# Performance work log

Measured on AMD Instinct MI355X. Metric: run time of the kernel, lower is better.

The kernel has to match this reference:

```python
import jax, jax.numpy as jnp
import numpy as np

B, T, D_MODEL, H, DK = 2, 1024, 1024, 16, 64
ADJ_TOPK, PHASE_TOPK, N_STEPS = 128, 128, 4


def _sparse_softmax(scores, k):
    # top-k per row, softmax over the kept entries, zeros elsewhere
    vals, idx = jax.lax.top_k(scores, k)            # (B,h,T,k)
    w = jax.nn.softmax(vals, axis=-1)
    b, h, t, _ = scores.shape
    bi = jnp.arange(b)[:, None, None, None]
    hi = jnp.arange(h)[None, :, None, None]
    ti = jnp.arange(t)[None, None, :, None]
    return jnp.zeros_like(scores).at[bi, hi, ti, idx].set(w)


def _heads(y):
    return y.reshape(B, T, H, DK).transpose(0, 2, 1, 3)  # (B,h,T,d_k)


def setup_inputs() -> dict:
    key = jax.random.key(0)
    ks = jax.random.split(key, 8)
    s = 0.02
    return {
        "x": jax.random.normal(ks[0], (B, T, D_MODEL), jnp.float32),
        "W_Q": jax.random.normal(ks[1], (D_MODEL, D_MODEL), jnp.float32) * s,
        "W_K": jax.random.normal(ks[2], (D_MODEL, D_MODEL), jnp.float32) * s,
        "W_re": jax.random.normal(ks[3], (D_MODEL, D_MODEL), jnp.float32) * s,
        "W_im": jax.random.normal(ks[4], (D_MODEL, D_MODEL), jnp.float32) * s,
        "W_V": jax.random.normal(ks[5], (D_MODEL, D_MODEL), jnp.float32) * s,
        "W_O": jax.random.normal(ks[6], (D_MODEL, D_MODEL), jnp.float32) * s,
        "logit_lam": jnp.float32(0.0),   # sigmoid -> lam=0.5
        "log_alpha": jnp.float32(-3.0),  # matches nn.Parameter init
    }


def reference(x, W_Q, W_K, W_re, W_im, W_V, W_O, logit_lam, log_alpha):
    # --- AdjacencyBuilder: A = sparse_softmax(QK^T/sqrt(dk)) ---
    Q = _heads(x @ W_Q.T)
    K = _heads(x @ W_K.T)
    scores = jnp.einsum('bhtd,bhsd->bhts', Q, K) / np.sqrt(DK).astype(np.float32)
    A = _sparse_softmax(scores, ADJ_TOPK)          # (B,h,T,T)

    # --- PhaseEncoding: D = W_re x + i W_im x (kept as real/imag pair) ---
    Dr = _heads(x @ W_re.T)
    Di = _heads(x @ W_im.T)
    D0r, D0i = Dr, Di

    # --- TopologyPropagation: D <- (1-lam) D + lam A D, n_steps times ---
    lam = jax.nn.sigmoid(logit_lam)
    for _ in range(N_STEPS):
        Dr = (1.0 - lam) * Dr + lam * jnp.einsum('bhts,bhsd->bhtd', A, Dr)
        Di = (1.0 - lam) * Di + lam * jnp.einsum('bhts,bhsd->bhtd', A, Di)
    alpha = jax.nn.sigmoid(log_alpha)
    Dr = Dr + alpha * D0r
    Di = Di + alpha * D0i

    # --- phase sync attention: Re(D_i . conj(D_j)) on unit-normalized D ---
    norm = jnp.maximum(jnp.sqrt(jnp.sum(Dr * Dr + Di * Di, axis=-1, keepdims=True)), 1e-6)
    Ur, Ui = Dr / norm, Di / norm
    phase_sim = (jnp.einsum('bhtd,bhsd->bhts', Ur, Ur)
                 + jnp.einsum('bhtd,bhsd->bhts', Ui, Ui)) * np.sqrt(2.0 * DK).astype(np.float32)
    phase_attn = _sparse_softmax(phase_sim, PHASE_TOPK)

    # --- weighted V sum + output projection ---
    V = _heads(x @ W_V.T)
    out = jnp.einsum('bhts,bhsd->bhtd', phase_attn, V)
    out = out.transpose(0, 2, 1, 3).reshape(B, T, D_MODEL)
    return out @ W_O.T, phase_attn
```

## Files before the change

kernel.cpp:

```cpp
#include <hip/hip_runtime.h>
#include <cstdint>
#include <cstddef>

#define B_  2
#define T_  1024
#define DM  1024
#define H_  16
#define DK_ 64
#define TOPK 128

typedef unsigned short ushort_t;
typedef __attribute__((ext_vector_type(8))) short short8;
typedef __attribute__((ext_vector_type(8))) unsigned short u16x8;
typedef __attribute__((ext_vector_type(4))) float f32x4;

__device__ __forceinline__ unsigned fkey16(unsigned b) {
  return (b & 0x8000u) ? (0xffffu & ~b) : (b | 0x8000u);
}

__device__ __forceinline__ ushort_t f2bf(float f) {
  unsigned u = __float_as_uint(f);
  return (ushort_t)((u + 0x7fffu + ((u >> 16) & 1u)) >> 16);
}
__device__ __forceinline__ float bf2f(ushort_t u) {
  return __uint_as_float((unsigned)u << 16);
}

__global__ __launch_bounds__(256) void cast_bf16_kernel(
    const float* __restrict__ in, ushort_t* __restrict__ out, int n4) {
  int i = blockIdx.x * 256 + threadIdx.x;
  if (i < n4) {
    float4 v = ((const float4*)in)[i];
    ushort4 o;
    o.x = f2bf(v.x); o.y = f2bf(v.y); o.z = f2bf(v.z); o.w = f2bf(v.w);
    ((ushort4*)out)[i] = o;
  }
}

template<int KDIM>
__device__ __forceinline__ void gemm_core(
    const ushort_t* __restrict__ Ab, const ushort_t* __restrict__ Bb,
    ushort_t* ldsA, ushort_t* ldsB, int tid, f32x4 acc[4][4]) {
  const int lane = tid & 63, wid = tid >> 6;
  const int wr = (wid >> 1) * 64, wc = (wid & 1) * 64;
  const int l15 = lane & 15, l4 = lane >> 4;
  for (int k0 = 0; k0 < KDIM; k0 += 64) {
    #pragma unroll
    for (int i = 0; i < 4; ++i) {
      int cid = tid + 256 * i;
      int row = cid >> 3, slot = cid & 7;
      int gc = slot ^ (row & 7);
      *(uint4*)&ldsA[row * 64 + slot * 8] =
          *(const uint4*)&Ab[(size_t)row * KDIM + k0 + gc * 8];
      *(uint4*)&ldsB[row * 64 + slot * 8] =
          *(const uint4*)&Bb[(size_t)row * KDIM + k0 + gc * 8];
    }
    __syncthreads();
    #pragma unroll
    for (int ks = 0; ks < 2; ++ks) {
      short8 af[4], bfr[4];
      #pragma unroll
      for (int m = 0; m < 4; ++m) {
        int r = wr + m * 16 + l15;
        int c = ks * 4 + l4;
        af[m] = *(const short8*)&ldsA[r * 64 + (c ^ (r & 7)) * 8];
      }
      #pragma unroll
      for (int n = 0; n < 4; ++n) {
        int r = wc + n * 16 + l15;
        int c = ks * 4 + l4;
        bfr[n] = *(const short8*)&ldsB[r * 64 + (c ^ (r & 7)) * 8];
      }
      #pragma unroll
      for (int m = 0; m < 4; ++m)
        #pragma unroll
        for (int n = 0; n < 4; ++n)
          acc[m][n] = __builtin_amdgcn_mfma_f32_16x16x32_bf16(
              af[m], bfr[n], acc[m][n], 0, 0, 0);
    }
    __syncthreads();
  }
}

__global__ __launch_bounds__(256) void proj5_mfma(
    const ushort_t* __restrict__ xb, const ushort_t* __restrict__ wb,
    ushort_t* __restrict__ qh_b, ushort_t* __restrict__ kh_b,
    ushort_t* __restrict__ dt0, ushort_t* __restrict__ vt_b) {
  __shared__ ushort_t ldsA[128 * 64];
  __shared__ ushort_t ldsB[128 * 64];
  int tid = threadIdx.x, z = blockIdx.z;
  const ushort_t* W = wb + (size_t)z * (DM * DM);
  f32x4 acc[4][4];
  #pragma unroll
  for (int m = 0; m < 4; ++m)
    #pragma unroll
    for (int n = 0; n < 4; ++n) acc[m][n] = (f32x4){0.f, 0.f, 0.f, 0.f};
  gemm_core<DM>(xb + (size_t)blockIdx.y * 128 * DM,
                W + (size_t)blockIdx.x * 128 * DM, ldsA, ldsB, tid, acc);
  const int lane = tid & 63, wid = tid >> 6;
  int row0 = blockIdx.y * 128 + (wid >> 1) * 64 + (lane >> 4) * 4;
  int col0 = blockIdx.x * 128 + (wid & 1) * 64 + (lane & 15);
  #pragma unroll
  for (int m = 0; m < 4; ++m)
    #pragma unroll
    for (int n = 0; n < 4; ++n)
      #pragma unroll
      for (int j = 0; j < 4; ++j) {
        int nr = row0 + m * 16 + j;
        int mc = col0 + n * 16;
        int b = nr >> 10, t = nr & 1023, h = mc >> 6, d = mc & 63;
        int head = b * H_ + h;
        float v = acc[m][n][j];
        if (z == 0) {
          qh_b[((size_t)head * T_ + t) * DK_ + d] = f2bf(v);
        } else if (z == 1) {
          kh_b[((size_t)head * T_ + t) * DK_ + d] = f2bf(v);
        } else if (z == 4) {
          vt_b[(size_t)head * 65536 + (size_t)d * 1024 + t] = f2bf(v);
        } else {
          int ddofs = (z == 3) ? 64 : 0;
          dt0[(size_t)head * 131072 + (size_t)(d + ddofs) * 1024 + t] = f2bf(v);
        }
      }
}

template<int KDIM, bool BF16OUT>
__global__ __launch_bounds__(256) void score_mfma(
    const ushort_t* __restrict__ A, const ushort_t* __restrict__ Bm,
    void* __restrict__ Sout, float scale) {
  __shared__ ushort_t ldsA[128 * 64];
  __shared__ ushort_t ldsB[128 * 64];
  int tid = threadIdx.x, z = blockIdx.z;
  f32x4 acc[4][4];
  #pragma unroll
  for (int m = 0; m < 4; ++m)
    #pragma unroll
    for (int n = 0; n < 4; ++n) acc[m][n] = (f32x4){0.f, 0.f, 0.f, 0.f};
  gemm_core<KDIM>(A + (size_t)z * T_ * KDIM + (size_t)blockIdx.y * 128 * KDIM,
                  Bm + (size_t)z * T_ * KDIM + (size_t)blockIdx.x * 128 * KDIM,
                  ldsA, ldsB, tid, acc);
  const int lane = tid & 63, wid = tid >> 6;
  int row0 = blockIdx.y * 128 + (wid >> 1) * 64 + (lane >> 4) * 4;
  int col0 = blockIdx.x * 128 + (wid & 1) * 64 + (lane & 15);
  if (BF16OUT) {
    ushort_t* Sz = (ushort_t*)Sout + (size_t)z * T_ * T_;
    #pragma unroll
    for (int m = 0; m < 4; ++m)
      #pragma unroll
      for (int n = 0; n < 4; ++n)
        #pragma unroll
        for (int j = 0; j < 4; ++j)
          Sz[(size_t)(row0 + m * 16 + j) * T_ + col0 + n * 16] =
              f2bf(acc[m][n][j] * scale);
  } else {
    float* Sz = (float*)Sout + (size_t)z * T_ * T_;
    #pragma unroll
    for (int m = 0; m < 4; ++m)
      #pragma unroll
      for (int n = 0; n < 4; ++n)
        #pragma unroll
        for (int j = 0; j < 4; ++j)
          Sz[(size_t)(row0 + m * 16 + j) * T_ + col0 + n * 16] =
              acc[m][n][j] * scale;
  }
}

__global__ __launch_bounds__(256) void prop_mfma(
    const ushort_t* __restrict__ Ab, const ushort_t* __restrict__ Dsrc,
    ushort_t* __restrict__ Ddst, const float* __restrict__ logit_lam) {
  __shared__ ushort_t ldsA[64 * 64];
  __shared__ ushort_t ldsB[128 * 64];
  int tid = threadIdx.x, hz = blockIdx.y;
  const int lane = tid & 63, wid = tid >> 6;
  const int wr = wid >> 1, wc = wid & 1;
  const int l15 = lane & 15, l4 = lane >> 4;
  const ushort_t* Ah = Ab + (size_t)hz * 1048576 + (size_t)blockIdx.x * 64 * 1024;
  const ushort_t* Dh = Dsrc + (size_t)hz * 131072;
  f32x4 acc[2][4];
  #pragma unroll
  for (int m = 0; m < 2; ++m)
    #pragma unroll
    for (int n = 0; n < 4; ++n) acc[m][n] = (f32x4){0.f, 0.f, 0.f, 0.f};
  for (int k0 = 0; k0 < 1024; k0 += 64) {
    #pragma unroll
    for (int i = 0; i < 2; ++i) {
      int cid = tid + 256 * i;
      int rowc = cid >> 3, slot = cid & 7;
      int gc = slot ^ (rowc & 7);
      *(uint4*)&ldsA[rowc * 64 + slot * 8] =
          *(const uint4*)&Ah[(size_t)rowc * 1024 + k0 + gc * 8];
    }
    #pragma unroll
    for (int i = 0; i < 4; ++i) {
      int cid = tid + 256 * i;
      int rowc = cid >> 3, slot = cid & 7;
      int gc = slot ^ (rowc & 7);
      *(uint4*)&ldsB[rowc * 64 + slot * 8] =
          *(const uint4*)&Dh[(size_t)rowc * 1024 + k0 + gc * 8];
    }
    __syncthreads();
    #pragma unroll
    for (int ks = 0; ks < 2; ++ks) {
      short8 af[2], bfr[4];
      #pragma unroll
      for (int m = 0; m < 2; ++m) {
        int r = wr * 32 + m * 16 + l15;
        int c = ks * 4 + l4;
        af[m] = *(const short8*)&ldsA[r * 64 + (c ^ (r & 7)) * 8];
      }
      #pragma unroll
      for (int n = 0; n < 4; ++n) {
        int r = wc * 64 + n * 16 + l15;
        int c = ks * 4 + l4;
        bfr[n] = *(const short8*)&ldsB[r * 64 + (c ^ (r & 7)) * 8];
      }
      #pragma unroll
      for (int m = 0; m < 2; ++m)
        #pragma unroll
        for (int n = 0; n < 4; ++n)
          acc[m][n] = __builtin_amdgcn_mfma_f32_16x16x32_bf16(
              af[m], bfr[n], acc[m][n], 0, 0, 0);
    }
    __syncthreads();
  }
  float lam = 1.f / (1.f + __expf(-logit_lam[0]));
  ushort_t* Dd = Ddst + (size_t)hz * 131072;
  #pragma unroll
  for (int m = 0; m < 2; ++m)
    #pragma unroll
    for (int n = 0; n < 4; ++n)
      #pragma unroll
      for (int j = 0; j < 4; ++j) {
        int t = blockIdx.x * 64 + wr * 32 + m * 16 + l4 * 4 + j;
        int dd = wc * 64 + n * 16 + l15;
        size_t o = (size_t)dd * 1024 + t;
        float oldv = bf2f(Dh[o]);
        Dd[o] = f2bf((1.f - lam) * oldv + lam * acc[m][n][j]);
      }
}

template<int MODE>
__global__ __launch_bounds__(256) void topk16_kernel(
    ushort_t* __restrict__ Sb, float* __restrict__ denseOut) {
  const int tid = threadIdx.x;
  const int lane = tid & 63, wv = tid >> 6;
  const int row = blockIdx.x * 4 + wv;
  ushort_t* Srow = Sb + (size_t)row * 1024;

  float scr[2][8];
  unsigned kk[2][8];
  #pragma unroll
  for (int g = 0; g < 2; ++g) {
    u16x8 v = *(const u16x8*)&Srow[g * 512 + lane * 8];
    #pragma unroll
    for (int e = 0; e < 8; ++e) {
      scr[g][e] = bf2f(v[e]);
      kk[g][e] = fkey16((unsigned)v[e]);
    }
  }

  unsigned prefix = 0, r = TOPK;
  #pragma unroll
  for (int b = 15; b >= 0; --b) {
    unsigned want = (prefix << 1) | 1u;
    unsigned cnt = 0;
    #pragma unroll
    for (int g = 0; g < 2; ++g)
      #pragma unroll
      for (int e = 0; e < 8; ++e)
        cnt += (unsigned)__popcll(__ballot((kk[g][e] >> b) == want));
    if (cnt >= r) prefix = want;
    else { prefix <<= 1; r -= cnt; }
  }
  const unsigned thr = prefix;

  float mx = -3.402823466e38f;
  #pragma unroll
  for (int g = 0; g < 2; ++g)
    #pragma unroll
    for (int e = 0; e < 8; ++e) mx = fmaxf(mx, scr[g][e]);
  #pragma unroll
  for (int off = 1; off < 64; off <<= 1) mx = fmaxf(mx, __shfl_xor(mx, off));

  const unsigned long long below = (1ull << lane) - 1ull;
  unsigned cum = 0;
  float w[2][8];
  float ps = 0.f;
  #pragma unroll
  for (int g = 0; g < 2; ++g) {
    unsigned long long bal[8];
    #pragma unroll
    for (int e = 0; e < 8; ++e) bal[e] = __ballot(kk[g][e] == thr);
    unsigned rb = cum;
    #pragma unroll
    for (int e = 0; e < 8; ++e) rb += (unsigned)__popcll(bal[e] & below);
    unsigned ownPrior = 0;
    #pragma unroll
    for (int e = 0; e < 8; ++e) {
      bool eq = (kk[g][e] == thr);
      bool sel = (kk[g][e] > thr) || (eq && (rb + ownPrior) < r);
      ownPrior += eq ? 1u : 0u;
      float ex = sel ? __expf(scr[g][e] - mx) : 0.f;
      w[g][e] = ex;
      ps += ex;
    }
    #pragma unroll
    for (int e = 0; e < 8; ++e) cum += (unsigned)__popcll(bal[e]);
  }
  float pss = ps;
  #pragma unroll
  for (int off = 1; off < 64; off <<= 1) pss += __shfl_xor(pss, off);
  const float inv = 1.f / pss;

  if (MODE == 0) {
    float* Drow = denseOut + (size_t)row * 1024;
    #pragma unroll
    for (int g = 0; g < 2; ++g) {
      *(float4*)&Drow[g * 512 + lane * 8] =
          make_float4(w[g][0] * inv, w[g][1] * inv, w[g][2] * inv, w[g][3] * inv);
      *(float4*)&Drow[g * 512 + lane * 8 + 4] =
          make_float4(w[g][4] * inv, w[g][5] * inv, w[g][6] * inv, w[g][7] * inv);
    }
  } else {
    #pragma unroll
    for (int g = 0; g < 2; ++g) {
      u16x8 o;
      #pragma unroll
      for (int e = 0; e < 8; ++e) o[e] = f2bf(w[g][e] * inv);
      *(u16x8*)&Srow[g * 512 + lane * 8] = o;
    }
  }
}

__global__ __launch_bounds__(256) void finalize_kernel(
    const ushort_t* __restrict__ Dt, const ushort_t* __restrict__ Dt0,
    ushort_t* __restrict__ P, const float* __restrict__ log_alpha) {
  __shared__ float lds[64][129];
  __shared__ float red[4][64];
  __shared__ float nrmi[64];
  int tid = threadIdx.x;
  int hz = blockIdx.y;
  int t0 = blockIdx.x * 64;
  size_t base = (size_t)hz * 131072 + t0;
  float alpha = 1.f / (1.f + __expf(-log_alpha[0]));
  #pragma unroll
  for (int i = 0; i < 32; ++i) {
    int eid = tid + i * 256;
    int dd = eid >> 6, t = eid & 63;
    size_t o = base + (size_t)dd * 1024 + t;
    lds[t][dd] = bf2f(Dt[o]) + alpha * bf2f(Dt0[o]);
  }
  __syncthreads();
  int t = tid & 63, q = tid >> 6;
  float s = 0.f;
  #pragma unroll
  for (int k = 0; k < 32; ++k) {
    float v = lds[t][q * 32 + k];
    s += v * v;
  }
  red[q][t] = s;
  __syncthreads();
  if (tid < 64) {
    float tot = red[0][tid] + red[1][tid] + red[2][tid] + red[3][tid];
    nrmi[tid] = 1.f / fmaxf(sqrtf(tot), 1e-6f);
  }
  __syncthreads();
  #pragma unroll
  for (int i = 0; i < 32; ++i) {
    int eid = tid + i * 256;
    int dd = eid & 127, tt = eid >> 7;
    P[((size_t)hz * 1024 + t0 + tt) * 128 + dd] = f2bf(lds[tt][dd] * nrmi[tt]);
  }
}

__global__ __launch_bounds__(256) void attnv_mfma(
    const float* __restrict__ Wf, const ushort_t* __restrict__ Vt,
    ushort_t* __restrict__ attn_b) {
  __shared__ ushort_t ldsA[64 * 64];
  __shared__ ushort_t ldsB[64 * 64];
  int tid = threadIdx.x, hz = blockIdx.y;
  const int lane = tid & 63, wid = tid >> 6;
  const int wr = wid >> 1, wc = wid & 1;
  const int l15 = lane & 15, l4 = lane >> 4;
  const float* Wh = Wf + (size_t)hz * 1048576 + (size_t)blockIdx.x * 64 * 1024;
  const ushort_t* Vh = Vt + (size_t)hz * 65536;
  f32x4 acc[2][2];
  #pragma unroll
  for (int m = 0; m < 2; ++m)
    #pragma unroll
    for (int n = 0; n < 2; ++n) acc[m][n] = (f32x4){0.f, 0.f, 0.f, 0.f};
  for (int k0 = 0; k0 < 1024; k0 += 64) {
    #pragma unroll
    for (int i = 0; i < 4; ++i) {
      int cid = tid + 256 * i;
      int rowc = cid >> 4, c4 = cid & 15;
      float4 v = *(const float4*)&Wh[(size_t)rowc * 1024 + k0 + c4 * 4];
      int c = c4 >> 1, half = c4 & 1;
      ushort4 o;
      o.x = f2bf(v.x); o.y = f2bf(v.y); o.z = f2bf(v.z); o.w = f2bf(v.w);
      *(ushort4*)&ldsA[rowc * 64 + (c ^ (rowc & 7)) * 8 + half * 4] = o;
    }
    #pragma unroll
    for (int i = 0; i < 2; ++i) {
      int cid = tid + 256 * i;
      int rowc = cid >> 3, slot = cid & 7;
      int gc = slot ^ (rowc & 7);
      *(uint4*)&ldsB[rowc * 64 + slot * 8] =
          *(const uint4*)&Vh[(size_t)rowc * 1024 + k0 + gc * 8];
    }
    __syncthreads();
    #pragma unroll
    for (int ks = 0; ks < 2; ++ks) {
      short8 af[2], bfr[2];
      #pragma unroll
      for (int m = 0; m < 2; ++m) {
        int r = wr * 32 + m * 16 + l15;
        int c = ks * 4 + l4;
        af[m] = *(const short8*)&ldsA[r * 64 + (c ^ (r & 7)) * 8];
      }
      #pragma unroll
      for (int n = 0; n < 2; ++n) {
        int r = wc * 32 + n * 16 + l15;
        int c = ks * 4 + l4;
        bfr[n] = *(const short8*)&ldsB[r * 64 + (c ^ (r & 7)) * 8];
      }
      #pragma unroll
      for (int m = 0; m < 2; ++m)
        #pragma unroll
        for (int n = 0; n < 2; ++n)
          acc[m][n] = __builtin_amdgcn_mfma_f32_16x16x32_bf16(
              af[m], bfr[n], acc[m][n], 0, 0, 0);
    }
    __syncthreads();
  }
  int b = hz >> 4, h = hz & 15;
  #pragma unroll
  for (int m = 0; m < 2; ++m)
    #pragma unroll
    for (int n = 0; n < 2; ++n)
      #pragma unroll
      for (int j = 0; j < 4; ++j) {
        int t = blockIdx.x * 64 + wr * 32 + m * 16 + l4 * 4 + j;
        int d = wc * 32 + n * 16 + l15;
        attn_b[((size_t)(b * T_ + t)) * DM + h * DK_ + d] = f2bf(acc[m][n][j]);
      }
}

extern "C" void kernel_launch(void* const* d_in, const int* in_sizes, int n_in,
                              void* d_out, int out_size, void* d_ws, size_t ws_size,
                              hipStream_t stream) {
  (void)in_sizes; (void)n_in; (void)out_size; (void)ws_size;
  const float* x         = (const float*)d_in[0];
  const float* wq        = (const float*)d_in[1];
  const float* wk        = (const float*)d_in[2];
  const float* wre       = (const float*)d_in[3];
  const float* wim       = (const float*)d_in[4];
  const float* wv        = (const float*)d_in[5];
  const float* wo        = (const float*)d_in[6];
  const float* logit_lam = (const float*)d_in[7];
  const float* log_alpha = (const float*)d_in[8];

  float* out   = (float*)d_out;
  float* dense = out + (size_t)B_ * T_ * DM;
  ushort_t* w5_b = (ushort_t*)dense;

  char* ws = (char*)d_ws;
  const size_t MB = (size_t)1 << 20;
  ushort_t* A_b  = (ushort_t*)(ws + 0 * MB);
  ushort_t* S2_b = A_b;
  ushort_t* dt0  = (ushort_t*)(ws + 64 * MB);
  ushort_t* dtA  = (ushort_t*)(ws + 72 * MB);
  ushort_t* P_b  = dtA;
  ushort_t* dtB  = (ushort_t*)(ws + 80 * MB);
  ushort_t* vt_b = (ushort_t*)(ws + 88 * MB);
  ushort_t* xb   = (ushort_t*)(ws + 92 * MB);
  ushort_t* attn_b = xb;
  ushort_t* qh_b = (ushort_t*)(ws + 96 * MB);
  ushort_t* wo_b = qh_b;
  ushort_t* kh_b = (ushort_t*)(ws + 100 * MB);

  const int rows = B_ * H_ * T_;

  cast_bf16_kernel<<<2048, 256, 0, stream>>>(x, xb, (B_ * T_ * DM) / 4);
  cast_bf16_kernel<<<1024, 256, 0, stream>>>(wq,  w5_b + 0 * DM * DM, DM * DM / 4);
  cast_bf16_kernel<<<1024, 256, 0, stream>>>(wk,  w5_b + 1 * (size_t)DM * DM, DM * DM / 4);
  cast_bf16_kernel<<<1024, 256, 0, stream>>>(wre, w5_b + 2 * (size_t)DM * DM, DM * DM / 4);
  cast_bf16_kernel<<<1024, 256, 0, stream>>>(wim, w5_b + 3 * (size_t)DM * DM, DM * DM / 4);
  cast_bf16_kernel<<<1024, 256, 0, stream>>>(wv,  w5_b + 4 * (size_t)DM * DM, DM * DM / 4);

  proj5_mfma<<<dim3(8, 16, 5), 256, 0, stream>>>(
      xb, w5_b, qh_b, kh_b, dt0, vt_b);

  score_mfma<64, true><<<dim3(8, 8, 32), 256, 0, stream>>>(
      qh_b, kh_b, A_b, 0.125f);
  cast_bf16_kernel<<<1024, 256, 0, stream>>>(wo, wo_b, DM * DM / 4);
  topk16_kernel<1><<<rows / 4, 256, 0, stream>>>(A_b, nullptr);

  prop_mfma<<<dim3(16, 32), 256, 0, stream>>>(A_b, dt0, dtA, logit_lam);
  prop_mfma<<<dim3(16, 32), 256, 0, stream>>>(A_b, dtA, dtB, logit_lam);
  prop_mfma<<<dim3(16, 32), 256, 0, stream>>>(A_b, dtB, dtA, logit_lam);
  prop_mfma<<<dim3(16, 32), 256, 0, stream>>>(A_b, dtA, dtB, logit_lam);

  finalize_kernel<<<dim3(16, 32), 256, 0, stream>>>(dtB, dt0, P_b, log_alpha);

  score_mfma<128, true><<<dim3(8, 8, 32), 256, 0, stream>>>(
      P_b, P_b, S2_b, 11.3137085f);
  topk16_kernel<0><<<rows / 4, 256, 0, stream>>>(S2_b, dense);

  attnv_mfma<<<dim3(16, 32), 256, 0, stream>>>(dense, vt_b, attn_b);
  score_mfma<DM, false><<<dim3(8, 16, 1), 256, 0, stream>>>(
      attn_b, wo_b, out, 1.0f);
}
```

Measured before the change: 405.4 us.

## Use direct global-to-LDS loads, merge cast launches, feed bf16 attention to attnv

GEMM tile loads in gemm_core, prop_mfma and attnv_mfma now go straight from global memory into LDS through global_load_lds, skipping the trip through registers. The six fp32-to-bf16 cast launches are merged into one 2D-grid kernel. The phase top-k kernel now always writes a bf16 copy of the sparse attention, and attnv reads that copy instead of the fp32 dense output, removing an fp32 read and its conversion. The direct LDS writes drop the per-thread XOR swizzle on the write side but keep the swizzled global addressing, so the layout relies on the hardware placing lanes contiguously.

```diff
diff --git a/kernel.cpp b/kernel.cpp
--- a/kernel.cpp
+++ b/kernel.cpp
@@ -24,6 +24,36 @@
 }
 __device__ __forceinline__ float bf2f(ushort_t u) {
   return __uint_as_float((unsigned)u << 16);
+}
+
+__device__ __forceinline__ void gload_lds16(const ushort_t* g, ushort_t* l) {
+  __builtin_amdgcn_global_load_lds(
+      (const __attribute__((address_space(1))) unsigned int*)(const void*)g,
+      (__attribute__((address_space(3))) unsigned int*)(void*)l, 16, 0, 0);
+}
+
+__global__ __launch_bounds__(256) void cast6_kernel(
+    const float* __restrict__ x, const float* __restrict__ wq,
+    const float* __restrict__ wk, const float* __restrict__ wre,
+    const float* __restrict__ wim, const float* __restrict__ wv,
+    ushort_t* __restrict__ xb, ushort_t* __restrict__ w5b) {
+  int z = blockIdx.y;
+  const float* src; ushort_t* dst; int n4;
+  switch (z) {
+    case 0: src = x;   dst = xb;                 n4 = 524288; break;
+    case 1: src = wq;  dst = w5b;                n4 = 262144; break;
+    case 2: src = wk;  dst = w5b + 1048576;      n4 = 262144; break;
+    case 3: src = wre; dst = w5b + 2097152;      n4 = 262144; break;
+    case 4: src = wim; dst = w5b + 3145728;      n4 = 262144; break;
+    default: src = wv; dst = w5b + 4194304;      n4 = 262144; break;
+  }
+  int i = blockIdx.x * 256 + threadIdx.x;
+  if (i < n4) {
+    float4 v = ((const float4*)src)[i];
+    ushort4 o;
+    o.x = f2bf(v.x); o.y = f2bf(v.y); o.z = f2bf(v.z); o.w = f2bf(v.w);
+    ((ushort4*)dst)[i] = o;
+  }
 }
 
 __global__ __launch_bounds__(256) void cast_bf16_kernel(
@@ -50,10 +80,8 @@
       int cid = tid + 256 * i;
       int row = cid >> 3, slot = cid & 7;
       int gc = slot ^ (row & 7);
-      *(uint4*)&ldsA[row * 64 + slot * 8] =
-          *(const uint4*)&Ab[(size_t)row * KDIM + k0 + gc * 8];
-      *(uint4*)&ldsB[row * 64 + slot * 8] =
-          *(const uint4*)&Bb[(size_t)row * KDIM + k0 + gc * 8];
+      gload_lds16(&Ab[(size_t)row * KDIM + k0 + gc * 8], &ldsA[cid * 8]);
+      gload_lds16(&Bb[(size_t)row * KDIM + k0 + gc * 8], &ldsB[cid * 8]);
     }
     __syncthreads();
     #pragma unroll
@@ -182,21 +210,22 @@
     #pragma unroll
     for (int n = 0; n < 4; ++n) acc[m][n] = (f32x4){0.f, 0.f, 0.f, 0.f};
   for (int k0 = 0; k0 < 1024; k0 += 64) {
-    #pragma unroll
-    for (int i = 0; i < 2; ++i) {
-      int cid = tid + 256 * i;
+    {
+      int cid = tid;
       int rowc = cid >> 3, slot = cid & 7;
       int gc = slot ^ (rowc & 7);
-      *(uint4*)&ldsA[rowc * 64 + slot * 8] =
-          *(const uint4*)&Ah[(size_t)rowc * 1024 + k0 + gc * 8];
+      gload_lds16(&Ah[(size_t)rowc * 1024 + k0 + gc * 8], &ldsA[cid * 8]);
+      cid = tid + 256;
+      rowc = cid >> 3; slot = cid & 7;
+      gc = slot ^ (rowc & 7);
+      gload_lds16(&Ah[(size_t)rowc * 1024 + k0 + gc * 8], &ldsA[cid * 8]);
     }
     #pragma unroll
     for (int i = 0; i < 4; ++i) {
       int cid = tid + 256 * i;
       int rowc = cid >> 3, slot = cid & 7;
       int gc = slot ^ (rowc & 7);
-      *(uint4*)&ldsB[rowc * 64 + slot * 8] =
-          *(const uint4*)&Dh[(size_t)rowc * 1024 + k0 + gc * 8];
+      gload_lds16(&Dh[(size_t)rowc * 1024 + k0 + gc * 8], &ldsB[cid * 8]);
     }
     __syncthreads();
     #pragma unroll
@@ -321,14 +350,13 @@
       *(float4*)&Drow[g * 512 + lane * 8 + 4] =
           make_float4(w[g][4] * inv, w[g][5] * inv, w[g][6] * inv, w[g][7] * inv);
     }
-  } else {
-    #pragma unroll
-    for (int g = 0; g < 2; ++g) {
-      u16x8 o;
-      #pragma unroll
-      for (int e = 0; e < 8; ++e) o[e] = f2bf(w[g][e] * inv);
-      *(u16x8*)&Srow[g * 512 + lane * 8] = o;
-    }
+  }
+  #pragma unroll
+  for (int g = 0; g < 2; ++g) {
+    u16x8 o;
+    #pragma unroll
+    for (int e = 0; e < 8; ++e) o[e] = f2bf(w[g][e] * inv);
+    *(u16x8*)&Srow[g * 512 + lane * 8] = o;
   }
 }
 
@@ -374,7 +402,7 @@
 }
 
 __global__ __launch_bounds__(256) void attnv_mfma(
-    const float* __restrict__ Wf, const ushort_t* __restrict__ Vt,
+    const ushort_t* __restrict__ Wb, const ushort_t* __restrict__ Vt,
     ushort_t* __restrict__ attn_b) {
   __shared__ ushort_t ldsA[64 * 64];
   __shared__ ushort_t ldsB[64 * 64];
@@ -382,7 +410,7 @@
   const int lane = tid & 63, wid = tid >> 6;
   const int wr = wid >> 1, wc = wid & 1;
   const int l15 = lane & 15, l4 = lane >> 4;
-  const float* Wh = Wf + (size_t)hz * 1048576 + (size_t)blockIdx.x * 64 * 1024;
+  const ushort_t* Wh = Wb + (size_t)hz * 1048576 + (size_t)blockIdx.x * 64 * 1024;
   const ushort_t* Vh = Vt + (size_t)hz * 65536;
   f32x4 acc[2][2];
   #pragma unroll
@@ -390,23 +418,19 @@
     #pragma unroll
     for (int n = 0; n < 2; ++n) acc[m][n] = (f32x4){0.f, 0.f, 0.f, 0.f};
   for (int k0 = 0; k0 < 1024; k0 += 64) {
-    #pragma unroll
-    for (int i = 0; i < 4; ++i) {
-      int cid = tid + 256 * i;
-      int rowc = cid >> 4, c4 = cid & 15;
-      float4 v = *(const float4*)&Wh[(size_t)rowc * 1024 + k0 + c4 * 4];
-      int c = c4 >> 1, half = c4 & 1;
-      ushort4 o;
-      o.x = f2bf(v.x); o.y = f2bf(v.y); o.z = f2bf(v.z); o.w = f2bf(v.w);
-      *(ushort4*)&ldsA[rowc * 64 + (c ^ (rowc & 7)) * 8 + half * 4] = o;
-    }
     #pragma unroll
     for (int i = 0; i < 2; ++i) {
       int cid = tid + 256 * i;
       int rowc = cid >> 3, slot = cid & 7;
       int gc = slot ^ (rowc & 7);
-      *(uint4*)&ldsB[rowc * 64 + slot * 8] =
-          *(const uint4*)&Vh[(size_t)rowc * 1024 + k0 + gc * 8];
+      gload_lds16(&Wh[(size_t)rowc * 1024 + k0 + gc * 8], &ldsA[cid * 8]);
+    }
+    #pragma unroll
+    for (int i = 0; i < 2; ++i) {
+      int cid = tid + 256 * i;
+      int rowc = cid >> 3, slot = cid & 7;
+      int gc = slot ^ (rowc & 7);
+      gload_lds16(&Vh[(size_t)rowc * 1024 + k0 + gc * 8], &ldsB[cid * 8]);
     }
     __syncthreads();
     #pragma unroll
@@ -481,12 +505,8 @@
 
   const int rows = B_ * H_ * T_;
 
-  cast_bf16_kernel<<<2048, 256, 0, stream>>>(x, xb, (B_ * T_ * DM) / 4);
-  cast_bf16_kernel<<<1024, 256, 0, stream>>>(wq,  w5_b + 0 * DM * DM, DM * DM / 4);
-  cast_bf16_kernel<<<1024, 256, 0, stream>>>(wk,  w5_b + 1 * (size_t)DM * DM, DM * DM / 4);
-  cast_bf16_kernel<<<1024, 256, 0, stream>>>(wre, w5_b + 2 * (size_t)DM * DM, DM * DM / 4);
-  cast_bf16_kernel<<<1024, 256, 0, stream>>>(wim, w5_b + 3 * (size_t)DM * DM, DM * DM / 4);
-  cast_bf16_kernel<<<1024, 256, 0, stream>>>(wv,  w5_b + 4 * (size_t)DM * DM, DM * DM / 4);
+  cast6_kernel<<<dim3(2048, 6), 256, 0, stream>>>(
+      x, wq, wk, wre, wim, wv, xb, w5_b);
 
   proj5_mfma<<<dim3(8, 16, 5), 256, 0, stream>>>(
       xb, w5_b, qh_b, kh_b, dt0, vt_b);
@@ -507,7 +527,7 @@
       P_b, P_b, S2_b, 11.3137085f);
   topk16_kernel<0><<<rows / 4, 256, 0, stream>>>(S2_b, dense);
 
-  attnv_mfma<<<dim3(16, 32), 256, 0, stream>>>(dense, vt_b, attn_b);
+  attnv_mfma<<<dim3(16, 32), 256, 0, stream>>>(S2_b, vt_b, attn_b);
   score_mfma<DM, false><<<dim3(8, 16, 1), 256, 0, stream>>>(
       attn_b, wo_b, out, 1.0f);
 }
```

Result: faster. 378.3 us (-6.7%).
